# Kernel tuning notes

Measured on AMD Instinct MI355X. Metric: run time of the kernel, lower is better.

## Reference

```python
import jax, jax.numpy as jnp
import numpy as np

# Config matching init_kwargs: input_shape=(C,T,H,W)=(512,32,14,14), window_size=9, n_heads=8
B, C, T, H, W = 2, 512, 32, 14, 14
N, K = 8, 9
CI = C // N              # per-head inter channels (64)
P = (K - 1) // 2         # symmetric temporal zero-pad so S == T


def setup_inputs() -> dict:
    key = jax.random.key(0)
    ks = jax.random.split(key, 7)
    s = 0.02
    return {
        "x":  jax.random.normal(ks[0], (B, C, T, H, W), jnp.float32),
        # per-head 1x1x1 conv (Linear3d) weights/biases, stacked over heads
        "Wq": jax.random.normal(ks[1], (N, CI, C), jnp.float32) * s,
        "bq": jax.random.normal(ks[2], (N, CI), jnp.float32) * s,
        "Wk": jax.random.normal(ks[3], (N, CI, C), jnp.float32) * s,
        "bk": jax.random.normal(ks[4], (N, CI), jnp.float32) * s,
        "Wv": jax.random.normal(ks[5], (N, CI, C), jnp.float32) * s,
        "bv": jax.random.normal(ks[6], (N, CI), jnp.float32) * s,
    }


def reference(x, Wq, bq, Wk, bk, Wv, bv):
    # x: (B, C, T, H, W). Dropout (p=0.25) is inference-mode identity.
    Bx, Cx, Tx, Hx, Wd = x.shape
    HW = Hx * Wd
    xf = x.reshape(Bx, Cx, Tx, HW)

    # Queries: every original frame is the center of its own window -> project x directly.
    q = jnp.einsum('bctp,nic->bnitp', xf, Wq) + bq[None, :, :, None, None]  # (B,N,ci,T,HW)

    # Keys/values on temporally zero-padded input (Pad3d gives S == T windows).
    xp = jnp.pad(xf, ((0, 0), (0, 0), (P, P), (0, 0)))  # (B,C,T+K-1,HW)
    k = jnp.einsum('bctp,nic->bnitp', xp, Wk) + bk[None, :, :, None, None]
    v = jnp.einsum('bctp,nic->bnitp', xp, Wv) + bv[None, :, :, None, None]

    # Sliding windows over padded time: window s covers padded frames s..s+K-1
    win = jnp.arange(Tx)[:, None] + jnp.arange(K)[None, :]  # (T,K)
    kw = k[:, :, :, win]  # (B,N,ci,T,K,HW)
    vw = v[:, :, :, win].reshape(Bx, N, CI, Tx, K * HW)

    # alpha[b,n,t,p,m] = sum_i q[b,n,i,t,p] * k_win[b,n,i,t,m]; softmax over keys m
    alpha = jnp.einsum('bnitp,bnitkm->bntpkm', q, kw).reshape(Bx, N, Tx, HW, K * HW)
    alpha = jax.nn.softmax(alpha, axis=-1)

    # y = alpha @ value -> (B,N,ci,T,HW); head concat is channel-major reshape
    y = jnp.einsum('bntpm,bnitm->bnitp', alpha, vw)
    z = y.reshape(Bx, Cx, Tx, Hx, Wd) + x  # residual
    return z
```

## Files before the change

### kernel.cpp

```cpp
#include <hip/hip_runtime.h>
#include <hip/hip_bf16.h>
#include <stdint.h>
#include <cstddef>

#define BB  2
#define CC  512
#define TT  32
#define HWP 196
#define NH  8
#define KWIN 9
#define CID 64
#define PPAD 4
#define TP  40
#define MTOT 12544
#define NTOT 1536
#define VSLOT 224
#define KPITCH 72
#define VPITCH 232
#define GPITCH 72
#define LOG2E 1.44269504f

typedef unsigned short u16;
typedef unsigned int   u32;
typedef __attribute__((ext_vector_type(8))) short short8;
typedef __attribute__((ext_vector_type(4))) float floatx4;

__device__ __forceinline__ u16 f2bf(float f) {
    u32 u = __float_as_uint(f);
    u32 r = (u + 0x7fffu + ((u >> 16) & 1u)) >> 16;
    return (u16)r;
}
__device__ __forceinline__ u32 pack2bf(float a, float b) {
    return (u32)f2bf(a) | ((u32)f2bf(b) << 16);
}
__device__ __forceinline__ u32 packtrunc(float a, float b) {
    return __builtin_amdgcn_perm(__float_as_uint(b), __float_as_uint(a), 0x07060302u);
}

__global__ __launch_bounds__(256) void convert_w(
    const float* __restrict__ Wq, const float* __restrict__ Wk,
    const float* __restrict__ Wv, u16* __restrict__ Wbf)
{
    int id = blockIdx.x * 256 + threadIdx.x;
    if (id >= NTOT * CC / 2) return;
    int c2 = id & 255;
    int oc = id >> 8;
    int kind = oc >> 9;
    int idx = oc & 511;
    const float* src = (kind == 0 ? Wq : (kind == 1 ? Wk : Wv)) + (size_t)idx * CC + c2 * 2;
    ((u32*)Wbf)[id] = pack2bf(src[0], src[1]);
}

__global__ __launch_bounds__(256) void transpose_x(
    const float* __restrict__ x, u16* __restrict__ xt)
{
    __shared__ float T[64 * 197];
    int bx = blockIdx.x;
    int ct = bx & 7; bx >>= 3;
    int t = bx & 31;
    int b = bx >> 5;
    int tid = threadIdx.x;
    const float* src = x + ((size_t)(b * CC + ct * 64) * TT + t) * HWP;
    for (int i = tid; i < 64 * HWP; i += 256) {
        int c = i / HWP;
        int p = i - c * HWP;
        T[c * 197 + p] = src[(size_t)c * (TT * HWP) + p];
    }
    __syncthreads();
    u16* dst = xt + (size_t)((b * TT + t) * HWP) * CC + ct * 64;
    for (int i = tid; i < HWP * 64; i += 256) {
        int p = i >> 6;
        int c = i & 63;
        dst[(size_t)p * CC + c] = f2bf(T[c * 197 + p]);
    }
}

__global__ __launch_bounds__(256) void pad_fill(
    const float* __restrict__ bk, const float* __restrict__ bv,
    u16* __restrict__ Kout, u16* __restrict__ Vtp)
{
    int id = blockIdx.x * 256 + threadIdx.x;
    const int kper = 2 * NH * 8 * HWP * 32;
    const int vper = 2 * NH * 8 * 64 * (VSLOT/2);
    if (id >= kper + vper) return;
    if (id < kper) {
        int i = id;
        int ci2 = i & 31; i >>= 5;
        int p = i % HWP;  i /= HWP;
        int fr = i & 7;   i >>= 3;
        int head = i & 7;
        int b = i >> 3;
        int tp = fr < 4 ? fr : fr + 32;
        const float* bias = bk + head * CID + ci2 * 2;
        size_t addr = (((size_t)(b * NH + head) * TP + tp) * HWP + p) * 32 + ci2;
        ((u32*)Kout)[addr] = pack2bf(bias[0], bias[1]);
    } else {
        int i = id - kper;
        int s2 = i % (VSLOT/2); i /= (VSLOT/2);
        int ci = i & 63; i >>= 6;
        int fr = i & 7;  i >>= 3;
        int head = i & 7;
        int b = i >> 3;
        int tp = fr < 4 ? fr : fr + 32;
        float bias = bv[head * CID + ci];
        size_t addr = (((size_t)(b * NH + head) * TP + tp) * 64 + ci) * (VSLOT/2) + s2;
        ((u32*)Vtp)[addr] = pack2bf(bias, bias);
    }
}

__global__ __launch_bounds__(512) void proj_gemm2(
    const u16* __restrict__ xt, const u16* __restrict__ Wbf,
    const float* __restrict__ bq, const float* __restrict__ bk,
    const float* __restrict__ bv,
    u16* __restrict__ Qout, u16* __restrict__ Kout, u16* __restrict__ Vplain)
{
    __shared__ u16 sA[128 * GPITCH];
    __shared__ u16 sB[256 * GPITCH];

    int bx = blockIdx.x;
    int nb = bx % 6;
    int mt = bx / 6;
    int tid = threadIdx.x;
    int wave = tid >> 6, lane = tid & 63, quad = lane >> 4, l15 = lane & 15;
    int wm = wave >> 2, wn = wave & 3;
    int mbase = mt * 128 + wm * 64;
    int nbase = nb * 256 + wn * 64;

    floatx4 acc[4][4];
    #pragma unroll
    for (int ms = 0; ms < 4; ms++)
        #pragma unroll
        for (int ns = 0; ns < 4; ns++)
            acc[ms][ns] = (floatx4){0.f, 0.f, 0.f, 0.f};

    const u16* agbase = xt + (size_t)(mt * 128) * CC;
    const u16* bgbase = Wbf + (size_t)(nb * 256) * CC;

    for (int kc = 0; kc < 8; kc++) {
        __syncthreads();
        #pragma unroll
        for (int it = 0; it < 2; it++) {
            int idx = it * 512 + tid;
            int row = idx >> 3, jj = idx & 7;
            uint4 v = *(const uint4*)(agbase + (size_t)row * CC + kc * 64 + jj * 8);
            *(uint4*)&sA[row * GPITCH + jj * 8] = v;
        }
        #pragma unroll
        for (int it = 0; it < 4; it++) {
            int idx = it * 512 + tid;
            int row = idx >> 3, jj = idx & 7;
            uint4 v = *(const uint4*)(bgbase + (size_t)row * CC + kc * 64 + jj * 8);
            *(uint4*)&sB[row * GPITCH + jj * 8] = v;
        }
        __syncthreads();

        #pragma unroll
        for (int kk = 0; kk < 2; kk++) {
            short8 af[4], bf[4];
            #pragma unroll
            for (int ms = 0; ms < 4; ms++)
                af[ms] = *(const short8*)&sA[(wm * 64 + ms * 16 + l15) * GPITCH + kk * 32 + quad * 8];
            #pragma unroll
            for (int ns = 0; ns < 4; ns++)
                bf[ns] = *(const short8*)&sB[(wn * 64 + ns * 16 + l15) * GPITCH + kk * 32 + quad * 8];
            #pragma unroll
            for (int ms = 0; ms < 4; ms++)
                #pragma unroll
                for (int ns = 0; ns < 4; ns++)
                    acc[ms][ns] = __builtin_amdgcn_mfma_f32_16x16x32_bf16(
                        af[ms], bf[ns], acc[ms][ns], 0, 0, 0);
        }
    }

    float biasv[4];
    #pragma unroll
    for (int ns = 0; ns < 4; ns++) {
        int n = nbase + ns * 16 + l15;
        int kind = n >> 9;
        int idx = n & 511;
        const float* bpb = kind == 0 ? bq : (kind == 1 ? bk : bv);
        biasv[ns] = bpb[idx];
    }

    #pragma unroll
    for (int ms = 0; ms < 4; ms++) {
        #pragma unroll
        for (int r = 0; r < 4; r++) {
            int m = mbase + ms * 16 + quad * 4 + r;
            int b = m / (TT * HWP);
            int rem = m - b * (TT * HWP);
            int t = rem / HWP;
            int p = rem - t * HWP;
            #pragma unroll
            for (int ns = 0; ns < 4; ns++) {
                int n = nbase + ns * 16 + l15;
                int kind = n >> 9;
                int idx = n & 511;
                int head = idx >> 6;
                int ci = idx & 63;
                float val = acc[ms][ns][r] + biasv[ns];
                if (kind == 0) {
                    Qout[(((size_t)(b * NH + head) * TT + t) * HWP + p) * CID + ci]
                        = f2bf(val * LOG2E);
                } else if (kind == 1) {
                    Kout[(((size_t)(b * NH + head) * TP + (t + PPAD)) * HWP + p) * CID + ci]
                        = f2bf(val);
                } else {
                    Vplain[(((size_t)(b * NH + head) * TT + t) * HWP + p) * CID + ci]
                        = f2bf(val);
                }
            }
        }
    }
}

__global__ __launch_bounds__(256) void v_reformat(
    const u16* __restrict__ Vplain, u16* __restrict__ Vtp)
{
    __shared__ u16 T[HWP * 66];
    int bx = blockIdx.x;
    int t = bx & 31;
    int slab = bx >> 5;
    int tid = threadIdx.x;
    const u32* src = (const u32*)(Vplain + ((size_t)slab * TT + t) * (HWP * CID));
    for (int i = tid; i < HWP * 32; i += 256) {
        int p = i >> 5, c2 = i & 31;
        u32 v = src[i];
        T[p * 66 + c2 * 2]     = (u16)(v & 0xffffu);
        T[p * 66 + c2 * 2 + 1] = (u16)(v >> 16);
    }
    __syncthreads();
    u32* dst = (u32*)(Vtp + ((size_t)slab * TP + (t + PPAD)) * (64 * VSLOT));
    for (int i = tid; i < 64 * 98; i += 256) {
        int ci = i / 98;
        int s2 = i - ci * 98;
        int s = s2 * 2;
        int s5 = s & 31;
        int p0 = (s & ~31) | (((s5 >> 2) & 1) << 4) | ((s5 >> 3) << 2) | (s5 & 3);
        u32 lo = T[p0 * 66 + ci];
        u32 hi = T[(p0 + 1) * 66 + ci];
        dst[ci * (VSLOT / 2) + s2] = lo | (hi << 16);
    }
}

__global__ __launch_bounds__(256, 2) void attn_mfma4(
    const float* __restrict__ x,
    const u16* __restrict__ Qb, const u16* __restrict__ Kb,
    const u16* __restrict__ Vtp, float* __restrict__ zout)
{
    __shared__ union {
        struct { u16 K[224 * KPITCH]; u16 V[64 * VPITCH]; } s;
        float eT[HWP * 66];
    } u;

    int i = blockIdx.x;
    int xcd = i & 7;
    int r = i >> 3;
    int slab = ((r >= 32) ? 8 : 0) | xcd;
    int t = r & 31;
    int b = slab >> 3, n = slab & 7;

    int tid = threadIdx.x;
    int wave = tid >> 6;
    int lane = tid & 63;
    int quad = lane >> 4, l15 = lane & 15;

    const size_t krow0 = (size_t)slab * (TP * HWP);
    const u16* vslab = Vtp + (size_t)slab * (TP * 64 * VSLOT);
    const float tmask = (quad == 0) ? 1.0f : 0.0f;

    short8 qf[4][2];
    #pragma unroll
    for (int j = 0; j < 4; j++) {
        int qrow = (wave + 4 * j) * 16 + l15;
        qrow = qrow < HWP ? qrow : (HWP - 1);
        const u16* qp = Qb + ((size_t)(slab * TT + t) * HWP + qrow) * CID;
        qf[j][0] = *(const short8*)(qp + quad * 8);
        qf[j][1] = *(const short8*)(qp + 32 + quad * 8);
    }

    floatx4 acc[4][4];
    floatx4 accl[4];
    #pragma unroll
    for (int j = 0; j < 4; j++) {
        #pragma unroll
        for (int cg = 0; cg < 4; cg++) acc[j][cg] = (floatx4){0.f, 0.f, 0.f, 0.f};
        accl[j] = (floatx4){0.f, 0.f, 0.f, 0.f};
    }

    union { u32 w[4]; short8 s; } ones;
    ones.w[0] = 0x3F803F80u; ones.w[1] = 0x3F803F80u;
    ones.w[2] = 0x3F803F80u; ones.w[3] = 0x3F803F80u;

    for (int f = 0; f < KWIN; f++) {
        int rbase = (t + f) * HWP;

        __syncthreads();
        {
            const u16* kfr0 = Kb + krow0 * CID;
            #pragma unroll
            for (int it = 0; it < 7; it++) {
                int idx = it * 256 + tid;
                int p = idx >> 3, jj = idx & 7;
                int grow = rbase + p;
                grow = grow < (TP * HWP) ? grow : (TP * HWP - 1);
                uint4 v = *(const uint4*)(kfr0 + (size_t)grow * CID + jj * 8);
                *(uint4*)&u.s.K[p * KPITCH + jj * 8] = v;
            }
        }
        {
            const u16* vfr = vslab + (size_t)(t + f) * (64 * VSLOT);
            #pragma unroll
            for (int it = 0; it < 7; it++) {
                int idx = it * 256 + tid;
                int ci = idx / 28, jj = idx - ci * 28;
                uint4 v = *(const uint4*)(vfr + ci * VSLOT + jj * 8);
                *(uint4*)&u.s.V[ci * VPITCH + jj * 8] = v;
            }
        }
        __syncthreads();

        for (int c = 0; c < 6; c++) {
            const u16* kp0 = &u.s.K[(c * 32 + l15) * KPITCH + quad * 8];
            short8 kf00 = *(const short8*)(kp0);
            short8 kf01 = *(const short8*)(kp0 + 32);
            const u16* kp1 = kp0 + 16 * KPITCH;
            short8 kf10 = *(const short8*)(kp1);
            short8 kf11 = *(const short8*)(kp1 + 32);
            const u16* vp = &u.s.V[l15 * VPITCH + c * 32 + quad * 8];
            short8 vf0 = *(const short8*)(vp);
            short8 vf1 = *(const short8*)(vp + 16 * VPITCH);
            short8 vf2 = *(const short8*)(vp + 32 * VPITCH);
            short8 vf3 = *(const short8*)(vp + 48 * VPITCH);

            #pragma unroll
            for (int j = 0; j < 4; j++) {
                floatx4 sc0 = (floatx4){0.f, 0.f, 0.f, 0.f};
                sc0 = __builtin_amdgcn_mfma_f32_16x16x32_bf16(kf00, qf[j][0], sc0, 0, 0, 0);
                sc0 = __builtin_amdgcn_mfma_f32_16x16x32_bf16(kf01, qf[j][1], sc0, 0, 0, 0);
                floatx4 sc1 = (floatx4){0.f, 0.f, 0.f, 0.f};
                sc1 = __builtin_amdgcn_mfma_f32_16x16x32_bf16(kf10, qf[j][0], sc1, 0, 0, 0);
                sc1 = __builtin_amdgcn_mfma_f32_16x16x32_bf16(kf11, qf[j][1], sc1, 0, 0, 0);

                union { u32 w[4]; short8 s; } pf;
                pf.w[0] = packtrunc(exp2f(sc0[0]), exp2f(sc0[1]));
                pf.w[1] = packtrunc(exp2f(sc0[2]), exp2f(sc0[3]));
                pf.w[2] = packtrunc(exp2f(sc1[0]), exp2f(sc1[1]));
                pf.w[3] = packtrunc(exp2f(sc1[2]), exp2f(sc1[3]));

                acc[j][0] = __builtin_amdgcn_mfma_f32_16x16x32_bf16(pf.s, vf0, acc[j][0], 0, 0, 0);
                acc[j][1] = __builtin_amdgcn_mfma_f32_16x16x32_bf16(pf.s, vf1, acc[j][1], 0, 0, 0);
                acc[j][2] = __builtin_amdgcn_mfma_f32_16x16x32_bf16(pf.s, vf2, acc[j][2], 0, 0, 0);
                acc[j][3] = __builtin_amdgcn_mfma_f32_16x16x32_bf16(pf.s, vf3, acc[j][3], 0, 0, 0);
                accl[j]   = __builtin_amdgcn_mfma_f32_16x16x32_bf16(pf.s, ones.s, accl[j], 0, 0, 0);
            }
        }

        {
            const u16* kp0 = &u.s.K[(192 + l15) * KPITCH + quad * 8];
            short8 kf00 = *(const short8*)(kp0);
            short8 kf01 = *(const short8*)(kp0 + 32);
            const u16* vp = &u.s.V[l15 * VPITCH + 192 + quad * 8];
            short8 vf0 = *(const short8*)(vp);
            short8 vf1 = *(const short8*)(vp + 16 * VPITCH);
            short8 vf2 = *(const short8*)(vp + 32 * VPITCH);
            short8 vf3 = *(const short8*)(vp + 48 * VPITCH);

            #pragma unroll
            for (int j = 0; j < 4; j++) {
                floatx4 sc0 = (floatx4){0.f, 0.f, 0.f, 0.f};
                sc0 = __builtin_amdgcn_mfma_f32_16x16x32_bf16(kf00, qf[j][0], sc0, 0, 0, 0);
                sc0 = __builtin_amdgcn_mfma_f32_16x16x32_bf16(kf01, qf[j][1], sc0, 0, 0, 0);

                union { u32 w[4]; short8 s; } pf;
                pf.w[0] = packtrunc(exp2f(sc0[0]) * tmask, exp2f(sc0[1]) * tmask);
                pf.w[1] = packtrunc(exp2f(sc0[2]) * tmask, exp2f(sc0[3]) * tmask);
                pf.w[2] = 0u;
                pf.w[3] = 0u;

                acc[j][0] = __builtin_amdgcn_mfma_f32_16x16x32_bf16(pf.s, vf0, acc[j][0], 0, 0, 0);
                acc[j][1] = __builtin_amdgcn_mfma_f32_16x16x32_bf16(pf.s, vf1, acc[j][1], 0, 0, 0);
                acc[j][2] = __builtin_amdgcn_mfma_f32_16x16x32_bf16(pf.s, vf2, acc[j][2], 0, 0, 0);
                acc[j][3] = __builtin_amdgcn_mfma_f32_16x16x32_bf16(pf.s, vf3, acc[j][3], 0, 0, 0);
                accl[j]   = __builtin_amdgcn_mfma_f32_16x16x32_bf16(pf.s, ones.s, accl[j], 0, 0, 0);
            }
        }
    }

    __syncthreads();
    #pragma unroll
    for (int j = 0; j < 4; j++) {
        int tg = wave + 4 * j;
        float il[4];
        #pragma unroll
        for (int rr = 0; rr < 4; rr++) il[rr] = 1.0f / accl[j][rr];
        #pragma unroll
        for (int cg = 0; cg < 4; cg++) {
            #pragma unroll
            for (int rr = 0; rr < 4; rr++) {
                int p = tg * 16 + quad * 4 + rr;
                if (p < HWP)
                    u.eT[p * 66 + cg * 16 + l15] = acc[j][cg][rr] * il[rr];
            }
        }
    }
    __syncthreads();

    if (tid < HWP) {
        size_t base = ((size_t)(b * CC + n * CID) * TT + t) * HWP + tid;
        for (int ci = 0; ci < 64; ci++) {
            size_t a = base + (size_t)ci * (TT * HWP);
            zout[a] = u.eT[tid * 66 + ci] + x[a];
        }
    }
}

extern "C" void kernel_launch(void* const* d_in, const int* in_sizes, int n_in,
                              void* d_out, int out_size, void* d_ws, size_t ws_size,
                              hipStream_t stream) {
    const float* x  = (const float*)d_in[0];
    const float* Wq = (const float*)d_in[1];
    const float* bq = (const float*)d_in[2];
    const float* Wk = (const float*)d_in[3];
    const float* bk = (const float*)d_in[4];
    const float* Wv = (const float*)d_in[5];
    const float* bv = (const float*)d_in[6];
    float* z = (float*)d_out;

    const size_t qElems   = (size_t)BB * NH * TT * HWP * CID;
    const size_t kElems   = (size_t)BB * NH * TP * HWP * CID;
    const size_t vtpElems = (size_t)BB * NH * TP * 64 * VSLOT;

    u16* Qw  = (u16*)d_ws;
    u16* Kw  = Qw + qElems;
    u16* Vtp = Kw + kElems;
    u16* Wb  = Vtp + vtpElems;
    u16* Xt  = (u16*)d_out;
    u16* Vpl = Xt + qElems;

    convert_w<<<(NTOT * CC / 2 + 255) / 256, 256, 0, stream>>>(Wq, Wk, Wv, Wb);
    transpose_x<<<BB * TT * 8, 256, 0, stream>>>(x, Xt);
    {
        const int kper = 2 * NH * 8 * HWP * 32;
        const int vper = 2 * NH * 8 * 64 * (VSLOT / 2);
        pad_fill<<<(kper + vper + 255) / 256, 256, 0, stream>>>(bk, bv, Kw, Vtp);
    }
    proj_gemm2<<<98 * 6, 512, 0, stream>>>(Xt, Wb, bq, bk, bv, Qw, Kw, Vpl);
    v_reformat<<<BB * NH * TT, 256, 0, stream>>>(Vpl, Vtp);
    attn_mfma4<<<512, 256, 0, stream>>>(x, Qw, Kw, Vtp, z);
}
```

Measured before the change: 264.6 us.

## Load K/V fragments directly from global into registers with double-buffered chunks

Removes the per-frame LDS staging of K and V tiles and the two block barriers per frame. Each wave now loads its MFMA K and V fragments straight from global memory (relying on L1/L2), with software double-buffering so the next chunk's loads are in flight while the current chunk computes. This trades LDS traffic and syncs for redundant global loads across the four waves (each wave reads the same K/V) and higher register pressure at 2 blocks/SM launch bounds.

Result: faster. 255.1 us (-3.6%).

```diff
diff --git a/kernel.cpp b/kernel.cpp
--- a/kernel.cpp
+++ b/kernel.cpp
@@ -15,8 +15,6 @@
 #define MTOT 12544
 #define NTOT 1536
 #define VSLOT 224
-#define KPITCH 72
-#define VPITCH 232
 #define GPITCH 72
 #define LOG2E 1.44269504f
 
@@ -248,10 +246,7 @@
     const u16* __restrict__ Qb, const u16* __restrict__ Kb,
     const u16* __restrict__ Vtp, float* __restrict__ zout)
 {
-    __shared__ union {
-        struct { u16 K[224 * KPITCH]; u16 V[64 * VPITCH]; } s;
-        float eT[HWP * 66];
-    } u;
+    __shared__ float eT[HWP * 66];
 
     int i = blockIdx.x;
     int xcd = i & 7;
@@ -265,7 +260,7 @@
     int lane = tid & 63;
     int quad = lane >> 4, l15 = lane & 15;
 
-    const size_t krow0 = (size_t)slab * (TP * HWP);
+    const u16* kfr0 = Kb + (size_t)slab * (TP * HWP) * CID;
     const u16* vslab = Vtp + (size_t)slab * (TP * 64 * VSLOT);
     const float tmask = (quad == 0) ? 1.0f : 0.0f;
 
@@ -292,102 +287,96 @@
     ones.w[0] = 0x3F803F80u; ones.w[1] = 0x3F803F80u;
     ones.w[2] = 0x3F803F80u; ones.w[3] = 0x3F803F80u;
 
+    #define KLOAD(c, D00, D01, D10, D11) do {                                    \
+        const u16* a0_ = kfr0 + (size_t)(rbase + (c) * 32 + l15) * CID + quad * 8;\
+        const u16* a1_ = a0_ + (size_t)16 * CID;                                 \
+        D00 = *(const short8*)a0_;  D01 = *(const short8*)(a0_ + 32);            \
+        D10 = *(const short8*)a1_;  D11 = *(const short8*)(a1_ + 32);            \
+    } while (0)
+
+    #define KLOADTAIL(D00, D01) do {                                             \
+        int g_ = rbase + 192 + l15;                                              \
+        g_ = g_ < (TP * HWP - 1) ? g_ : (TP * HWP - 1);                          \
+        const u16* a0_ = kfr0 + (size_t)g_ * CID + quad * 8;                     \
+        D00 = *(const short8*)a0_;  D01 = *(const short8*)(a0_ + 32);            \
+    } while (0)
+
+    #define VLOAD(c, D0, D1, D2, D3) do {                                        \
+        const u16* v_ = vfr + l15 * VSLOT + (c) * 32 + quad * 8;                 \
+        D0 = *(const short8*)v_;                                                 \
+        D1 = *(const short8*)(v_ + 16 * VSLOT);                                  \
+        D2 = *(const short8*)(v_ + 32 * VSLOT);                                  \
+        D3 = *(const short8*)(v_ + 48 * VSLOT);                                  \
+    } while (0)
+
+    #define CHUNK_FULL(K00, K01, K10, K11, V0, V1, V2, V3)                       \
+        _Pragma("unroll")                                                        \
+        for (int j = 0; j < 4; j++) {                                            \
+            floatx4 sc0 = (floatx4){0.f, 0.f, 0.f, 0.f};                         \
+            sc0 = __builtin_amdgcn_mfma_f32_16x16x32_bf16(K00, qf[j][0], sc0, 0, 0, 0); \
+            sc0 = __builtin_amdgcn_mfma_f32_16x16x32_bf16(K01, qf[j][1], sc0, 0, 0, 0); \
+            floatx4 sc1 = (floatx4){0.f, 0.f, 0.f, 0.f};                         \
+            sc1 = __builtin_amdgcn_mfma_f32_16x16x32_bf16(K10, qf[j][0], sc1, 0, 0, 0); \
+            sc1 = __builtin_amdgcn_mfma_f32_16x16x32_bf16(K11, qf[j][1], sc1, 0, 0, 0); \
+            union { u32 w[4]; short8 s; } pf;                                    \
+            pf.w[0] = packtrunc(exp2f(sc0[0]), exp2f(sc0[1]));                   \
+            pf.w[1] = packtrunc(exp2f(sc0[2]), exp2f(sc0[3]));                   \
+            pf.w[2] = packtrunc(exp2f(sc1[0]), exp2f(sc1[1]));                   \
+            pf.w[3] = packtrunc(exp2f(sc1[2]), exp2f(sc1[3]));                   \
+            acc[j][0] = __builtin_amdgcn_mfma_f32_16x16x32_bf16(pf.s, V0, acc[j][0], 0, 0, 0); \
+            acc[j][1] = __builtin_amdgcn_mfma_f32_16x16x32_bf16(pf.s, V1, acc[j][1], 0, 0, 0); \
+            acc[j][2] = __builtin_amdgcn_mfma_f32_16x16x32_bf16(pf.s, V2, acc[j][2], 0, 0, 0); \
+            acc[j][3] = __builtin_amdgcn_mfma_f32_16x16x32_bf16(pf.s, V3, acc[j][3], 0, 0, 0); \
+            accl[j]   = __builtin_amdgcn_mfma_f32_16x16x32_bf16(pf.s, ones.s, accl[j], 0, 0, 0); \
+        }
+
+    #define CHUNK_TAIL(K00, K01, V0, V1, V2, V3)                                 \
+        _Pragma("unroll")                                                        \
+        for (int j = 0; j < 4; j++) {                                            \
+            floatx4 sc0 = (floatx4){0.f, 0.f, 0.f, 0.f};                         \
+            sc0 = __builtin_amdgcn_mfma_f32_16x16x32_bf16(K00, qf[j][0], sc0, 0, 0, 0); \
+            sc0 = __builtin_amdgcn_mfma_f32_16x16x32_bf16(K01, qf[j][1], sc0, 0, 0, 0); \
+            union { u32 w[4]; short8 s; } pf;                                    \
+            pf.w[0] = packtrunc(exp2f(sc0[0]) * tmask, exp2f(sc0[1]) * tmask);   \
+            pf.w[1] = packtrunc(exp2f(sc0[2]) * tmask, exp2f(sc0[3]) * tmask);   \
+            pf.w[2] = 0u;                                                        \
+            pf.w[3] = 0u;                                                        \
+            acc[j][0] = __builtin_amdgcn_mfma_f32_16x16x32_bf16(pf.s, V0, acc[j][0], 0, 0, 0); \
+            acc[j][1] = __builtin_amdgcn_mfma_f32_16x16x32_bf16(pf.s, V1, acc[j][1], 0, 0, 0); \
+            acc[j][2] = __builtin_amdgcn_mfma_f32_16x16x32_bf16(pf.s, V2, acc[j][2], 0, 0, 0); \
+            acc[j][3] = __builtin_amdgcn_mfma_f32_16x16x32_bf16(pf.s, V3, acc[j][3], 0, 0, 0); \
+            accl[j]   = __builtin_amdgcn_mfma_f32_16x16x32_bf16(pf.s, ones.s, accl[j], 0, 0, 0); \
+        }
+
     for (int f = 0; f < KWIN; f++) {
         int rbase = (t + f) * HWP;
-
-        __syncthreads();
-        {
-            const u16* kfr0 = Kb + krow0 * CID;
-            #pragma unroll
-            for (int it = 0; it < 7; it++) {
-                int idx = it * 256 + tid;
-                int p = idx >> 3, jj = idx & 7;
-                int grow = rbase + p;
-                grow = grow < (TP * HWP) ? grow : (TP * HWP - 1);
-                uint4 v = *(const uint4*)(kfr0 + (size_t)grow * CID + jj * 8);
-                *(uint4*)&u.s.K[p * KPITCH + jj * 8] = v;
-            }
-        }
-        {
-            const u16* vfr = vslab + (size_t)(t + f) * (64 * VSLOT);
-            #pragma unroll
-            for (int it = 0; it < 7; it++) {
-                int idx = it * 256 + tid;
-                int ci = idx / 28, jj = idx - ci * 28;
-                uint4 v = *(const uint4*)(vfr + ci * VSLOT + jj * 8);
-                *(uint4*)&u.s.V[ci * VPITCH + jj * 8] = v;
-            }
-        }
-        __syncthreads();
-
-        for (int c = 0; c < 6; c++) {
-            const u16* kp0 = &u.s.K[(c * 32 + l15) * KPITCH + quad * 8];
-            short8 kf00 = *(const short8*)(kp0);
-            short8 kf01 = *(const short8*)(kp0 + 32);
-            const u16* kp1 = kp0 + 16 * KPITCH;
-            short8 kf10 = *(const short8*)(kp1);
-            short8 kf11 = *(const short8*)(kp1 + 32);
-            const u16* vp = &u.s.V[l15 * VPITCH + c * 32 + quad * 8];
-            short8 vf0 = *(const short8*)(vp);
-            short8 vf1 = *(const short8*)(vp + 16 * VPITCH);
-            short8 vf2 = *(const short8*)(vp + 32 * VPITCH);
-            short8 vf3 = *(const short8*)(vp + 48 * VPITCH);
-
-            #pragma unroll
-            for (int j = 0; j < 4; j++) {
-                floatx4 sc0 = (floatx4){0.f, 0.f, 0.f, 0.f};
-                sc0 = __builtin_amdgcn_mfma_f32_16x16x32_bf16(kf00, qf[j][0], sc0, 0, 0, 0);
-                sc0 = __builtin_amdgcn_mfma_f32_16x16x32_bf16(kf01, qf[j][1], sc0, 0, 0, 0);
-                floatx4 sc1 = (floatx4){0.f, 0.f, 0.f, 0.f};
-                sc1 = __builtin_amdgcn_mfma_f32_16x16x32_bf16(kf10, qf[j][0], sc1, 0, 0, 0);
-                sc1 = __builtin_amdgcn_mfma_f32_16x16x32_bf16(kf11, qf[j][1], sc1, 0, 0, 0);
-
-                union { u32 w[4]; short8 s; } pf;
-                pf.w[0] = packtrunc(exp2f(sc0[0]), exp2f(sc0[1]));
-                pf.w[1] = packtrunc(exp2f(sc0[2]), exp2f(sc0[3]));
-                pf.w[2] = packtrunc(exp2f(sc1[0]), exp2f(sc1[1]));
-                pf.w[3] = packtrunc(exp2f(sc1[2]), exp2f(sc1[3]));
-
-                acc[j][0] = __builtin_amdgcn_mfma_f32_16x16x32_bf16(pf.s, vf0, acc[j][0], 0, 0, 0);
-                acc[j][1] = __builtin_amdgcn_mfma_f32_16x16x32_bf16(pf.s, vf1, acc[j][1], 0, 0, 0);
-                acc[j][2] = __builtin_amdgcn_mfma_f32_16x16x32_bf16(pf.s, vf2, acc[j][2], 0, 0, 0);
-                acc[j][3] = __builtin_amdgcn_mfma_f32_16x16x32_bf16(pf.s, vf3, acc[j][3], 0, 0, 0);
-                accl[j]   = __builtin_amdgcn_mfma_f32_16x16x32_bf16(pf.s, ones.s, accl[j], 0, 0, 0);
-            }
-        }
-
-        {
-            const u16* kp0 = &u.s.K[(192 + l15) * KPITCH + quad * 8];
-            short8 kf00 = *(const short8*)(kp0);
-            short8 kf01 = *(const short8*)(kp0 + 32);
-            const u16* vp = &u.s.V[l15 * VPITCH + 192 + quad * 8];
-            short8 vf0 = *(const short8*)(vp);
-            short8 vf1 = *(const short8*)(vp + 16 * VPITCH);
-            short8 vf2 = *(const short8*)(vp + 32 * VPITCH);
-            short8 vf3 = *(const short8*)(vp + 48 * VPITCH);
-
-            #pragma unroll
-            for (int j = 0; j < 4; j++) {
-                floatx4 sc0 = (floatx4){0.f, 0.f, 0.f, 0.f};
-                sc0 = __builtin_amdgcn_mfma_f32_16x16x32_bf16(kf00, qf[j][0], sc0, 0, 0, 0);
-                sc0 = __builtin_amdgcn_mfma_f32_16x16x32_bf16(kf01, qf[j][1], sc0, 0, 0, 0);
-
-                union { u32 w[4]; short8 s; } pf;
-                pf.w[0] = packtrunc(exp2f(sc0[0]) * tmask, exp2f(sc0[1]) * tmask);
-                pf.w[1] = packtrunc(exp2f(sc0[2]) * tmask, exp2f(sc0[3]) * tmask);
-                pf.w[2] = 0u;
-                pf.w[3] = 0u;
-
-                acc[j][0] = __builtin_amdgcn_mfma_f32_16x16x32_bf16(pf.s, vf0, acc[j][0], 0, 0, 0);
-                acc[j][1] = __builtin_amdgcn_mfma_f32_16x16x32_bf16(pf.s, vf1, acc[j][1], 0, 0, 0);
-                acc[j][2] = __builtin_amdgcn_mfma_f32_16x16x32_bf16(pf.s, vf2, acc[j][2], 0, 0, 0);
-                acc[j][3] = __builtin_amdgcn_mfma_f32_16x16x32_bf16(pf.s, vf3, acc[j][3], 0, 0, 0);
-                accl[j]   = __builtin_amdgcn_mfma_f32_16x16x32_bf16(pf.s, ones.s, accl[j], 0, 0, 0);
-            }
-        }
-    }
-
-    __syncthreads();
+        const u16* vfr = vslab + (size_t)(t + f) * (64 * VSLOT);
+
+        short8 ka00, ka01, ka10, ka11, kb00, kb01, kb10, kb11;
+        short8 va0, va1, va2, va3, vb0, vb1, vb2, vb3;
+
+        KLOAD(0, ka00, ka01, ka10, ka11);  VLOAD(0, va0, va1, va2, va3);
+        KLOAD(1, kb00, kb01, kb10, kb11);  VLOAD(1, vb0, vb1, vb2, vb3);
+        CHUNK_FULL(ka00, ka01, ka10, ka11, va0, va1, va2, va3);
+        KLOAD(2, ka00, ka01, ka10, ka11);  VLOAD(2, va0, va1, va2, va3);
+        CHUNK_FULL(kb00, kb01, kb10, kb11, vb0, vb1, vb2, vb3);
+        KLOAD(3, kb00, kb01, kb10, kb11);  VLOAD(3, vb0, vb1, vb2, vb3);
+        CHUNK_FULL(ka00, ka01, ka10, ka11, va0, va1, va2, va3);
+        KLOAD(4, ka00, ka01, ka10, ka11);  VLOAD(4, va0, va1, va2, va3);
+        CHUNK_FULL(kb00, kb01, kb10, kb11, vb0, vb1, vb2, vb3);
+        KLOAD(5, kb00, kb01, kb10, kb11);  VLOAD(5, vb0, vb1, vb2, vb3);
+        CHUNK_FULL(ka00, ka01, ka10, ka11, va0, va1, va2, va3);
+        KLOADTAIL(ka00, ka01);             VLOAD(6, va0, va1, va2, va3);
+        CHUNK_FULL(kb00, kb01, kb10, kb11, vb0, vb1, vb2, vb3);
+        CHUNK_TAIL(ka00, ka01, va0, va1, va2, va3);
+    }
+
+    #undef KLOAD
+    #undef KLOADTAIL
+    #undef VLOAD
+    #undef CHUNK_FULL
+    #undef CHUNK_TAIL
+
     #pragma unroll
     for (int j = 0; j < 4; j++) {
         int tg = wave + 4 * j;
@@ -400,7 +389,7 @@
             for (int rr = 0; rr < 4; rr++) {
                 int p = tg * 16 + quad * 4 + rr;
                 if (p < HWP)
-                    u.eT[p * 66 + cg * 16 + l15] = acc[j][cg][rr] * il[rr];
+                    eT[p * 66 + cg * 16 + l15] = acc[j][cg][rr] * il[rr];
             }
         }
     }
@@ -410,7 +399,7 @@
         size_t base = ((size_t)(b * CC + n * CID) * TT + t) * HWP + tid;
         for (int ci = 0; ci < 64; ci++) {
             size_t a = base + (size_t)ci * (TT * HWP);
-            zout[a] = u.eT[tid * 66 + ci] + x[a];
+            zout[a] = eT[tid * 66 + ci] + x[a];
         }
     }
 }
```
